# Kernel tuning notes

Measured on AMD Instinct MI355X. Metric: run time of the kernel, lower is better.

The kernel has to match this reference:

```python
import jax, jax.numpy as jnp
import numpy as np

B, N, D, M, L = 64, 4096, 128, 1024, 128  # batch, set size, d_in, num_ref_points, num_projections


def setup_inputs() -> dict:
    key = jax.random.key(0)
    k1, k2, k3, k4 = jax.random.split(key, 4)
    X = jax.random.normal(k1, (B, N, D), dtype=jnp.float32)
    theta_v = jax.random.normal(k2, (L, D), dtype=jnp.float32)          # weight_norm 'v' param
    ref_points = jax.random.normal(k3, (M, L), dtype=jnp.float32)       # self.reference
    weight = jax.random.normal(k4, (L, M), dtype=jnp.float32) * 0.04    # xavier-ish self.weight
    return {"X": X, "theta_v": theta_v, "ref_points": ref_points, "weight": weight}


def reference(X, theta_v, ref_points, weight):
    # weight_norm(dim=0) with g fixed to 1: effective row-normalized projection matrix
    W = theta_v / jnp.linalg.norm(theta_v, axis=1, keepdims=True)       # [L, D]
    slices = jnp.einsum('bnd,ld->bnl', X, W)                            # [B, N, L]
    s = jnp.sort(slices, axis=1)                                        # sort each slice over the set dim

    # M != N: linear interp of sorted values onto the M-point grid (torchinterp1d equivalent;
    # xnew range is strictly inside x range since M < N, so clamping never triggers)
    x = jnp.linspace(0.0, 1.0, N + 2)[1:-1]                             # [N]
    xnew = jnp.linspace(0.0, 1.0, M + 2)[1:-1]                          # [M]
    y = jnp.transpose(s, (0, 2, 1)).reshape(B * L, N)                   # [B*L, N]
    interp = jax.vmap(lambda yr: jnp.interp(xnew, x, yr))(y)            # [B*L, M]
    interp = jnp.transpose(interp.reshape(B, L, M), (0, 2, 1))          # [B, M, L]

    # gather interpolated quantiles by the sort order of the reference set
    Rind = jnp.argsort(ref_points, axis=0)                              # [M, L]
    gathered = jnp.take_along_axis(interp, jnp.broadcast_to(Rind[None], (B, M, L)), axis=1)
    diff = ref_points[None, :, :] - gathered                            # [B, M, L]

    # weighted sum over reference points per projection
    return jnp.einsum('bml,lm->bl', diff, weight)                       # [B, L]
```

## Files before the change

### kernel.cpp

```cpp
#include <hip/hip_runtime.h>

static constexpr int Bc = 64;
static constexpr int Nc = 4096;
static constexpr int Dc = 128;
static constexpr int Mc = 1024;
static constexpr int Lc = 128;

using short8   = __attribute__((ext_vector_type(8))) short;
using ushort8v = __attribute__((ext_vector_type(8))) unsigned short;
using f32x4    = __attribute__((ext_vector_type(4))) float;

__device__ __forceinline__ unsigned short f2bf(float x) {
  unsigned u = __builtin_bit_cast(unsigned, x);
  return (unsigned short)((u + 0x7FFFu + ((u >> 16) & 1u)) >> 16);
}
__device__ __forceinline__ float bf2f(unsigned short h) {
  unsigned u = ((unsigned)h) << 16;
  return __builtin_bit_cast(float, u);
}

__device__ __forceinline__ int swz(int i) { return i ^ ((i >> 4) & 31); }

__global__ __launch_bounds__(256) void setup_kernel(
    const float* __restrict__ theta_v, const float* __restrict__ ref,
    const float* __restrict__ weight, unsigned short* __restrict__ Wh,
    unsigned short* __restrict__ Wl, float* __restrict__ C,
    float* __restrict__ v) {
  constexpr int NBv = 2048;
  constexpr float LOv = -4.2f;
  constexpr float SCv = (float)NBv / 8.4f;

  __shared__ int pref[NBv];
  __shared__ float skey[Mc];
  __shared__ unsigned short sidx[Mc];
  __shared__ float vrow[Nc];
  __shared__ int wsum[4];
  __shared__ float s2[2];
  __shared__ float c4[4];

  int l = blockIdx.x;
  int tid = threadIdx.x;
  int lane = tid & 63, wv = tid >> 6;

  float x[4];
  #pragma unroll
  for (int j = 0; j < 4; ++j) x[j] = ref[(size_t)(tid + 256 * j) * Lc + l];

  for (int i = tid; i < NBv; i += 256) pref[i] = 0;
  for (int i = tid; i < Nc; i += 256) vrow[i] = 0.f;

  float wval = 0.f;
  if (tid < Dc) {
    wval = theta_v[l * Dc + tid];
    float sq = wval * wval;
    #pragma unroll
    for (int off = 1; off < 64; off <<= 1) sq += __shfl_xor(sq, off, 64);
    if (lane == 0) s2[wv] = sq;
  }
  {
    float cacc = 0.f;
    #pragma unroll
    for (int j = 0; j < 4; ++j) cacc += x[j] * weight[(size_t)l * Mc + tid + 256 * j];
    #pragma unroll
    for (int off = 1; off < 64; off <<= 1) cacc += __shfl_xor(cacc, off, 64);
    if (lane == 0) c4[wv] = cacc;
  }
  __syncthreads();

  if (tid < Dc) {
    float norm = sqrtf(s2[0] + s2[1]);
    float val = wval / norm;
    unsigned short hi = f2bf(val);
    Wh[l * Dc + tid] = hi;
    Wl[l * Dc + tid] = f2bf(val - bf2f(hi));
  }
  if (tid == 0) C[l] = c4[0] + c4[1] + c4[2] + c4[3];

  int bb[4];
  #pragma unroll
  for (int j = 0; j < 4; ++j) {
    int bi = (int)((x[j] - LOv) * SCv);
    bi = bi < 0 ? 0 : (bi > NBv - 1 ? NBv - 1 : bi);
    bb[j] = bi;
    atomicAdd(&pref[swz(bi)], 1);
  }
  __syncthreads();

  {
    int base_ = tid * 8;
    int loc[8]; int s = 0;
    #pragma unroll
    for (int j = 0; j < 8; ++j) loc[j] = pref[swz(base_ + j)];
    #pragma unroll
    for (int j = 0; j < 8; ++j) { int c = loc[j]; loc[j] = s; s += c; }
    int inc = s;
    #pragma unroll
    for (int off = 1; off < 64; off <<= 1) {
      int o = __shfl_up(inc, off, 64);
      if (lane >= off) inc += o;
    }
    if (lane == 63) wsum[wv] = inc;
    __syncthreads();
    int wbase = 0;
    #pragma unroll
    for (int ww = 0; ww < 4; ++ww) if (ww < wv) wbase += wsum[ww];
    int tbase = wbase + inc - s;
    #pragma unroll
    for (int j = 0; j < 8; ++j) pref[swz(base_ + j)] = tbase + loc[j];
  }
  __syncthreads();

  #pragma unroll
  for (int j = 0; j < 4; ++j) {
    int p = atomicAdd(&pref[swz(bb[j])], 1);
    skey[p] = x[j];
    sidx[p] = (unsigned short)(tid + 256 * j);
  }
  __syncthreads();

  #pragma unroll
  for (int k = 0; k < 4; ++k) {
    int p = tid + 256 * k;
    float y = skey[p];
    int m = sidx[p];
    int b = (int)((y - LOv) * SCv);
    b = b < 0 ? 0 : (b > NBv - 1 ? NBv - 1 : b);
    int lo_ = b ? pref[swz(b - 1)] : 0;
    int hi_ = pref[swz(b)];
    int r = lo_;
    for (int q = lo_; q < hi_; ++q) {
      float z = skey[q];
      r += (z < y || (z == y && sidx[q] < m)) ? 1 : 0;
    }
    float wvv = weight[(size_t)l * Mc + r];
    double pos = (double)(m + 1) * (double)(Nc + 1) / (double)(Mc + 1) - 1.0;
    int i0 = (int)pos;
    float t = (float)(pos - (double)i0);
    atomicAdd(&vrow[i0], (1.0f - t) * wvv);
    atomicAdd(&vrow[i0 + 1], t * wvv);
  }
  __syncthreads();
  for (int i = tid; i < Nc; i += 256) v[(size_t)l * Nc + i] = vrow[i];
}

__global__ __launch_bounds__(512) void gemm_kernel(
    const float* __restrict__ X, const unsigned short* __restrict__ Whp,
    const unsigned short* __restrict__ Wlp, float* __restrict__ sl) {
  __shared__ unsigned short Bh[2][128][40];
  __shared__ unsigned short Bl[2][128][40];

  int bloc = blockIdx.y;
  int nbase = blockIdx.x * 128;
  int tid = threadIdx.x;
  int lane = tid & 63;
  int wv = tid >> 6;
  int m16 = lane & 15;
  int kg = lane >> 4;

  int brow = tid >> 2;
  int bc = (tid & 3) * 8;
  const unsigned short* gbh = Whp + (size_t)brow * Dc + bc;
  const unsigned short* gbl = Wlp + (size_t)brow * Dc + bc;

  const float* arow = X + ((size_t)bloc * Nc + nbase + wv * 16 + m16) * Dc + kg * 8;
  float4 af[4][2];
  #pragma unroll
  for (int c = 0; c < 4; ++c) {
    af[c][0] = *(const float4*)(arow + c * 32);
    af[c][1] = *(const float4*)(arow + c * 32 + 4);
  }

  ushort8v rbh = *(const ushort8v*)gbh;
  ushort8v rbl = *(const ushort8v*)gbl;
  *(ushort8v*)&Bh[0][brow][bc] = rbh;
  *(ushort8v*)&Bl[0][brow][bc] = rbl;
  rbh = *(const ushort8v*)(gbh + 32);
  rbl = *(const ushort8v*)(gbl + 32);

  f32x4 acc[8] = {};
  __syncthreads();

  #pragma unroll
  for (int c = 0; c < 4; ++c) {
    if (c < 3) {
      *(ushort8v*)&Bh[(c + 1) & 1][brow][bc] = rbh;
      *(ushort8v*)&Bl[(c + 1) & 1][brow][bc] = rbl;
    }
    if (c < 2) {
      rbh = *(const ushort8v*)(gbh + (c + 2) * 32);
      rbl = *(const ushort8v*)(gbl + (c + 2) * 32);
    }

    float xs[8] = {af[c][0].x, af[c][0].y, af[c][0].z, af[c][0].w,
                   af[c][1].x, af[c][1].y, af[c][1].z, af[c][1].w};
    short8 ah, al;
    #pragma unroll
    for (int e = 0; e < 8; ++e) {
      unsigned short h = f2bf(xs[e]);
      ah[e] = (short)h;
      al[e] = (short)f2bf(xs[e] - bf2f(h));
    }

    #pragma unroll
    for (int u = 0; u < 8; ++u) {
      short8 bh = *(const short8*)&Bh[c & 1][u * 16 + m16][kg * 8];
      short8 bl = *(const short8*)&Bl[c & 1][u * 16 + m16][kg * 8];
      acc[u] = __builtin_amdgcn_mfma_f32_16x16x32_bf16(ah, bh, acc[u], 0, 0, 0);
      acc[u] = __builtin_amdgcn_mfma_f32_16x16x32_bf16(ah, bl, acc[u], 0, 0, 0);
      acc[u] = __builtin_amdgcn_mfma_f32_16x16x32_bf16(al, bh, acc[u], 0, 0, 0);
    }
    __syncthreads();
  }

  #pragma unroll
  for (int u = 0; u < 8; ++u) {
    int l = u * 16 + m16;
    int n0 = nbase + wv * 16 + kg * 4;
    float* dst = sl + ((size_t)bloc * Lc + l) * Nc + n0;
    *(float4*)dst = *(float4*)&acc[u];
  }
}

__device__ __forceinline__ int gbin(float x) {
  constexpr int NB = 4096;
  float t = __builtin_amdgcn_exp2f(x * -2.45541f);
  float r = __builtin_amdgcn_rcpf(1.0f + t);
  int bi = (int)((float)NB * r);
  return bi < 0 ? 0 : (bi > NB - 1 ? NB - 1 : bi);
}

__global__ __launch_bounds__(512, 8) void rank_dot_kernel(
    const float* __restrict__ sl, const float* __restrict__ v,
    const float* __restrict__ C, float* __restrict__ out, int b0) {
  constexpr int NB = 4096;
  constexpr int NT = 512;
  constexpr int EL = Nc / NT;

  __shared__ int pref[NB];
  __shared__ float skey[Nc];
  int* wsum = (int*)skey;
  float* red = (float*)pref;

  int l = blockIdx.x & (Lc - 1);
  int bloc = blockIdx.x >> 7;
  int tid = threadIdx.x;
  const float* src = sl + ((size_t)bloc * Lc + l) * Nc;

  float x[EL];
  {
    const float4* s4 = (const float4*)src;
    #pragma unroll
    for (int j = 0; j < EL / 4; ++j) {
      float4 f = s4[tid + NT * j];
      x[j * 4 + 0] = f.x; x[j * 4 + 1] = f.y;
      x[j * 4 + 2] = f.z; x[j * 4 + 3] = f.w;
    }
  }

  for (int i = tid; i < NB; i += NT) pref[i] = 0;
  __syncthreads();

  int bb[EL];
  int ofs[EL];
  #pragma unroll
  for (int j = 0; j < EL; ++j) {
    int bi = gbin(x[j]);
    bb[j] = bi;
    ofs[j] = atomicAdd(&pref[swz(bi)], 1);
  }
  __syncthreads();

  {
    int base_ = tid * 8;
    int loc[8]; int s = 0;
    #pragma unroll
    for (int j = 0; j < 8; ++j) loc[j] = pref[swz(base_ + j)];
    #pragma unroll
    for (int j = 0; j < 8; ++j) { int c = loc[j]; loc[j] = s; s += c; }
    int lane = tid & 63, wvv = tid >> 6;
    int inc = s;
    #pragma unroll
    for (int off = 1; off < 64; off <<= 1) {
      int o = __shfl_up(inc, off, 64);
      if (lane >= off) inc += o;
    }
    if (lane == 63) wsum[wvv] = inc;
    __syncthreads();
    int wbase = 0;
    #pragma unroll
    for (int ww = 0; ww < 8; ++ww) if (ww < wvv) wbase += wsum[ww];
    int tbase = wbase + inc - s;
    #pragma unroll
    for (int j = 0; j < 8; ++j) pref[swz(base_ + j)] = tbase + loc[j];
  }
  __syncthreads();

  #pragma unroll
  for (int j = 0; j < EL; ++j) {
    skey[pref[swz(bb[j])] + ofs[j]] = x[j];
  }
  __syncthreads();

  const float* vrow = v + (size_t)l * Nc;
  float acc = 0.f;
  #pragma unroll
  for (int k = 0; k < EL; ++k) {
    int p = tid + NT * k;
    float y = skey[p];
    int b = gbin(y);
    int lo_ = pref[swz(b)];
    int hi_ = (b == NB - 1) ? Nc : pref[swz(b + 1)];
    int r = lo_;
    for (int q = lo_; q < hi_; ++q) {
      float z = skey[q];
      r += (z < y || (z == y && q < p)) ? 1 : 0;
    }
    acc += y * vrow[r];
  }

  #pragma unroll
  for (int off = 1; off < 64; off <<= 1) acc += __shfl_xor(acc, off, 64);
  __syncthreads();
  if ((tid & 63) == 0) red[tid >> 6] = acc;
  __syncthreads();
  if (tid == 0) {
    float t = 0.f;
    #pragma unroll
    for (int ww = 0; ww < 8; ++ww) t += red[ww];
    int b = b0 + bloc;
    out[(size_t)b * Lc + l] = C[l] - t;
  }
}

extern "C" void kernel_launch(void* const* d_in, const int* in_sizes, int n_in,
                              void* d_out, int out_size, void* d_ws, size_t ws_size,
                              hipStream_t stream) {
  const float* X       = (const float*)d_in[0];
  const float* theta_v = (const float*)d_in[1];
  const float* ref     = (const float*)d_in[2];
  const float* weight  = (const float*)d_in[3];
  float* out = (float*)d_out;

  float* v  = (float*)d_ws;
  unsigned short* Wh = (unsigned short*)(v + (size_t)Lc * Nc);
  unsigned short* Wl = Wh + (size_t)Lc * Dc;
  float* Cc = (float*)(Wl + (size_t)Lc * Dc);
  float* sl = Cc + 128;
  size_t used = (size_t)((char*)sl - (char*)d_ws);
  size_t per_b = (size_t)Lc * Nc * sizeof(float);
  int chunk = 1;
  if (ws_size > used + per_b) {
    size_t c = (ws_size - used) / per_b;
    chunk = (int)(c > (size_t)Bc ? (size_t)Bc : c);
    if (chunk < 1) chunk = 1;
  }

  setup_kernel<<<Lc, 256, 0, stream>>>(theta_v, ref, weight, Wh, Wl, Cc, v);

  for (int b0 = 0; b0 < Bc; b0 += chunk) {
    int nb = (Bc - b0) < chunk ? (Bc - b0) : chunk;
    dim3 g1(Nc / 128, nb);
    gemm_kernel<<<g1, 512, 0, stream>>>(X + (size_t)b0 * Nc * Dc, Wh, Wl, sl);
    rank_dot_kernel<<<(size_t)nb * Lc, 512, 0, stream>>>(sl, v, Cc, out, b0);
  }
}
```

Measured before the change: 152.9 us.

## Finish bucket sort with per-bin insertion sort, then do a contiguous vectorized dot product

Replaces the per-element rank computation (which scanned each element's histogram bin and gathered from v at a random rank) with an in-place insertion sort inside each bin, one thread per eight bins. After that the shared keys are fully sorted, so the weighted sum becomes a contiguous float4 dot product against the v row. This removes the gather and the repeated rank scans, but the thread-to-bin assignment can load-imbalance when bins are skewed, and the sort adds a barrier.

```diff
diff --git a/kernel.cpp b/kernel.cpp
--- a/kernel.cpp
+++ b/kernel.cpp
@@ -237,7 +237,7 @@
   constexpr int EL = Nc / NT;
 
   __shared__ int pref[NB];
-  __shared__ float skey[Nc];
+  __shared__ __align__(16) float skey[Nc];
   int* wsum = (int*)skey;
   float* red = (float*)pref;
 
@@ -301,21 +301,39 @@
   }
   __syncthreads();
 
-  const float* vrow = v + (size_t)l * Nc;
-  float acc = 0.f;
-  #pragma unroll
-  for (int k = 0; k < EL; ++k) {
-    int p = tid + NT * k;
-    float y = skey[p];
-    int b = gbin(y);
-    int lo_ = pref[swz(b)];
-    int hi_ = (b == NB - 1) ? Nc : pref[swz(b + 1)];
-    int r = lo_;
-    for (int q = lo_; q < hi_; ++q) {
-      float z = skey[q];
-      r += (z < y || (z == y && q < p)) ? 1 : 0;
-    }
-    acc += y * vrow[r];
+  {
+    int base = tid * 8;
+    int cur = pref[swz(base)];
+    #pragma unroll
+    for (int i = 0; i < 8; ++i) {
+      int bidx = base + i + 1;
+      int nxt = (bidx < NB) ? pref[swz(bidx)] : Nc;
+      for (int ii = cur + 1; ii < nxt; ++ii) {
+        float key = skey[ii];
+        int j = ii - 1;
+        while (j >= cur) {
+          float z = skey[j];
+          if (z <= key) break;
+          skey[j + 1] = z;
+          --j;
+        }
+        skey[j + 1] = key;
+      }
+      cur = nxt;
+    }
+  }
+  __syncthreads();
+
+  const f32x4* skey4 = (const f32x4*)skey;
+  const f32x4* vrow4 = (const f32x4*)(v + (size_t)l * Nc);
+  float acc;
+  {
+    f32x4 a0 = skey4[tid];
+    f32x4 w0 = vrow4[tid];
+    f32x4 a1 = skey4[tid + NT];
+    f32x4 w1 = vrow4[tid + NT];
+    acc = a0[0] * w0[0] + a0[1] * w0[1] + a0[2] * w0[2] + a0[3] * w0[3]
+        + a1[0] * w1[0] + a1[1] * w1[1] + a1[2] * w1[2] + a1[3] * w1[3];
   }
 
   #pragma unroll
```

Result: slower. 194.8 us (+27.4%).
